# Kernel optimization log

Measured on AMD Instinct MI355X. Metric: run time of the kernel, lower is better.

Reference implementation:

```python
import jax, jax.numpy as jnp
import numpy as np

CLAMP_LO, CLAMP_HI, CLAMP_GATE_MAX = -10.0, 10.0, 10.0
E, TOPK = 8, 2
M, K, N = 2048, 2048, 1408  # tokens, hidden_dim, intermediate_dim
CAPACITY = 2 * (M * TOPK // E)


def setup_inputs() -> dict:
    key = jax.random.key(0)
    ks = jax.random.split(key, 6)
    bk = 1.0 / np.sqrt(K)  # kaiming_uniform(a=sqrt(5)) bound = 1/sqrt(fan_in)
    bn = 1.0 / np.sqrt(N)
    return {
        "flat_h": jax.random.normal(ks[0], (M, K), jnp.float32),
        "flat_idx": jax.random.randint(ks[1], (M, TOPK), 0, E),
        "flat_gate": jax.random.uniform(ks[2], (M, TOPK), jnp.float32),
        "gate_weight": jax.random.uniform(ks[3], (E, N, K), jnp.float32, -bk, bk),
        "up_weight": jax.random.uniform(ks[4], (E, N, K), jnp.float32, -bk, bk),
        "down_weight": jax.random.uniform(ks[5], (E, K, N), jnp.float32, -bn, bn),
    }


def reference(flat_h, flat_idx, flat_gate, gate_weight, up_weight, down_weight):
    m, top_k = flat_idx.shape
    k = flat_h.shape[1]
    e = gate_weight.shape[0]
    r = m * top_k

    expert_id = flat_idx.reshape(-1)                                   # (R,)
    gate = flat_gate.reshape(-1)                                       # (R,)
    token_index = jnp.repeat(jnp.arange(m, dtype=jnp.int32), top_k)    # (R,)

    # stable sort rows by expert id (mirrors torch.argsort(..., stable=True))
    sort_idx = jnp.argsort(expert_id, stable=True)
    sorted_eid = expert_id[sort_idx]
    tok_sorted = token_index[sort_idx]
    gate_sorted = gate[sort_idx]

    # position of each sorted row inside its expert group
    counts = jnp.bincount(expert_id, length=e)
    starts = jnp.concatenate([jnp.zeros(1, counts.dtype), jnp.cumsum(counts)[:-1]])
    pos = jnp.arange(r) - starts[sorted_eid]                           # (R,)

    # dispatch: scatter sorted tokens into fixed-capacity (E, C, K) buffer
    buf = jnp.zeros((e, CAPACITY, k), flat_h.dtype)
    buf = buf.at[sorted_eid, pos].set(flat_h[tok_sorted])

    # grouped GEMMs: weights stored (E, out, in) like nn.Linear
    g = jnp.einsum("eck,enk->ecn", buf, gate_weight)
    g = jnp.minimum(g, CLAMP_GATE_MAX)
    u = jnp.clip(jnp.einsum("eck,enk->ecn", buf, up_weight), CLAMP_LO, CLAMP_HI)
    h = jax.nn.silu(g) * u                                             # SwiGLU (E, C, N)
    d = jnp.einsum("ecn,ekn->eck", h, down_weight)                     # (E, C, K)

    # combine: gather each routed row back, weight by gate, sum over top_k slots
    expert_out = d[sorted_eid, pos]                                    # (R, K)
    weighted = expert_out * gate_sorted[:, None]
    out = jnp.zeros((m, k), flat_h.dtype).at[tok_sorted].add(weighted)
    return out
```

## Files before the change

### kernel.cpp

```cpp
#include <hip/hip_runtime.h>
#include <hip/hip_bf16.h>

#define M_TOK 2048
#define KDIM 2048
#define NDIM 1408
#define NEXP 8
#define RROWS (M_TOK * 2)
#define CAP 1024

typedef __attribute__((ext_vector_type(8))) short short8;
typedef __attribute__((ext_vector_type(4))) float f32x4;

__device__ __forceinline__ unsigned short bf16rn(float f) {
    unsigned int u = __builtin_bit_cast(unsigned int, f);
    u += 0x7FFFu + ((u >> 16) & 1u);
    return (unsigned short)(u >> 16);
}
__device__ __forceinline__ unsigned int pk2(float a, float b) {
    return (unsigned int)bf16rn(a) | ((unsigned int)bf16rn(b) << 16);
}
__device__ __forceinline__ unsigned int cvtpk(float a, float b) {
    __hip_bfloat162 h = __float22bfloat162_rn(make_float2(a, b));
    unsigned int u;
    __builtin_memcpy(&u, &h, 4);
    return u;
}

__device__ __forceinline__ void glds16(const void* g, void* l) {
    __builtin_amdgcn_global_load_lds(
        (const __attribute__((address_space(1))) unsigned int*)g,
        (__attribute__((address_space(3))) unsigned int*)l, 16, 0, 0);
}

__global__ void k_route(const float* __restrict__ h, const int* __restrict__ idx,
                        int* __restrict__ cnt, int* __restrict__ slot_of,
                        unsigned short* __restrict__ bufA) {
    int r = blockIdx.x;
    __shared__ int s_ep;
    if (threadIdx.x == 0) {
        int e = idx[r];
        int p = atomicAdd(&cnt[e], 1);
        int ep = e * CAP + p;
        slot_of[r] = ep;
        s_ep = ep;
    }
    __syncthreads();
    int ep = s_ep;
    const float4* src = (const float4*)(h + (size_t)(r >> 1) * KDIM) + threadIdx.x * 2;
    float4 a = src[0], b = src[1];
    uint4 o;
    o.x = pk2(a.x, a.y); o.y = pk2(a.z, a.w);
    o.z = pk2(b.x, b.y); o.w = pk2(b.z, b.w);
    *((uint4*)(bufA + (size_t)ep * KDIM) + threadIdx.x) = o;
}

__global__ __launch_bounds__(256, 2)
void k_gemm1(const unsigned short* __restrict__ bufA,
             const float* __restrict__ gw,
             const float* __restrict__ uw,
             const int* __restrict__ cnt, unsigned short* __restrict__ hbuf) {
    const int f = blockIdx.x;
    const int e = f & 7;
    const int t = f >> 3;
    const int n_blk = t % 11;
    const int m_blk = t / 11;
    const int m0 = m_blk * 128;
    if (m0 >= cnt[e]) return;
    const int n0 = n_blk * 128;

    const unsigned short* A = bufA + (size_t)e * CAP * KDIM;
    const float* G = gw + (size_t)e * NDIM * KDIM;
    const float* U = uw + (size_t)e * NDIM * KDIM;

    __shared__ unsigned short sA[128 * 64];
    __shared__ unsigned short sG[128 * 64];
    __shared__ unsigned short sU[128 * 64];

    const int tid = threadIdx.x;
    const int lane = tid & 63;
    const int wave = tid >> 6;
    const int wm = (wave >> 1) * 64, wn = (wave & 1) * 64;
    const int q = lane >> 4, l15 = lane & 15;
    const int sr = lane >> 3;
    const int scb = (lane & 7) ^ (sr & 7);
    const int xi = l15 & 7;
    const int cbl0 = (q ^ xi) * 8;
    const int cbl1 = ((4 + q) ^ xi) * 8;

    const int wrow = tid >> 1;
    const int wh = tid & 1;
    const int wx = wrow & 7;
    const float* gsrc0 = G + (size_t)(n0 + wrow) * KDIM + wh * 32;
    const float* usrc0 = U + (size_t)(n0 + wrow) * KDIM + wh * 32;
    unsigned short* wdG = &sG[wrow * 64];
    unsigned short* wdU = &sU[wrow * 64];

    f32x4 accG[4][4] = {};
    f32x4 accU[4][4] = {};

    for (int k0 = 0; k0 < KDIM; k0 += 64) {
        const float4* gs = (const float4*)(gsrc0 + k0);
        const float4* us = (const float4*)(usrc0 + k0);
        float4 gv[8], uv[8];
#pragma unroll
        for (int i = 0; i < 8; i++) gv[i] = gs[i];
#pragma unroll
        for (int i = 0; i < 8; i++) uv[i] = us[i];

        __syncthreads();
#pragma unroll
        for (int c = 0; c < 4; c++) {
            int seg = wave * 4 + c;
            int row = seg * 8 + sr;
            glds16(A + (size_t)(m0 + row) * KDIM + k0 + scb * 8, &sA[seg * 512]);
        }
#pragma unroll
        for (int g = 0; g < 4; g++) {
            uint4 o;
            o.x = cvtpk(gv[2 * g].x, gv[2 * g].y);
            o.y = cvtpk(gv[2 * g].z, gv[2 * g].w);
            o.z = cvtpk(gv[2 * g + 1].x, gv[2 * g + 1].y);
            o.w = cvtpk(gv[2 * g + 1].z, gv[2 * g + 1].w);
            *(uint4*)(wdG + (((wh * 4 + g) ^ wx) * 8)) = o;
        }
#pragma unroll
        for (int g = 0; g < 4; g++) {
            uint4 o;
            o.x = cvtpk(uv[2 * g].x, uv[2 * g].y);
            o.y = cvtpk(uv[2 * g].z, uv[2 * g].w);
            o.z = cvtpk(uv[2 * g + 1].x, uv[2 * g + 1].y);
            o.w = cvtpk(uv[2 * g + 1].z, uv[2 * g + 1].w);
            *(uint4*)(wdU + (((wh * 4 + g) ^ wx) * 8)) = o;
        }
        __syncthreads();

#pragma unroll
        for (int kh = 0; kh < 2; kh++) {
            const int co = kh ? cbl1 : cbl0;
            short8 af[4], gf[4], uf[4];
#pragma unroll
            for (int i = 0; i < 4; i++) {
                af[i] = *(const short8*)&sA[(wm + i * 16 + l15) * 64 + co];
                gf[i] = *(const short8*)&sG[(wn + i * 16 + l15) * 64 + co];
                uf[i] = *(const short8*)&sU[(wn + i * 16 + l15) * 64 + co];
            }
#pragma unroll
            for (int i = 0; i < 4; i++)
#pragma unroll
                for (int j = 0; j < 4; j++) {
                    accG[i][j] = __builtin_amdgcn_mfma_f32_16x16x32_bf16(af[i], gf[j], accG[i][j], 0, 0, 0);
                    accU[i][j] = __builtin_amdgcn_mfma_f32_16x16x32_bf16(af[i], uf[j], accU[i][j], 0, 0, 0);
                }
        }
    }

    unsigned short* H = hbuf + (size_t)e * CAP * NDIM;
#pragma unroll
    for (int i = 0; i < 4; i++)
#pragma unroll
        for (int j = 0; j < 4; j++) {
            int col = n0 + wn + j * 16 + l15;
#pragma unroll
            for (int rg = 0; rg < 4; rg++) {
                int row = m0 + wm + i * 16 + q * 4 + rg;
                float g = accG[i][j][rg];
                float u = accU[i][j][rg];
                g = fminf(g, 10.f);
                u = fminf(fmaxf(u, -10.f), 10.f);
                float hv = g / (1.f + __expf(-g)) * u;
                H[(size_t)row * NDIM + col] = bf16rn(hv);
            }
        }
}

__global__ __launch_bounds__(256, 2)
void k_gemm2(const unsigned short* __restrict__ hbuf,
             const float* __restrict__ dwn, const int* __restrict__ cnt,
             float* __restrict__ dbuf) {
    const int f = blockIdx.x;
    const int e = f & 7;
    const int t = f >> 3;
    const int n_blk = t & 15;
    const int m_blk = t >> 4;
    const int cnt_e = cnt[e];
    const int m0 = m_blk * 128;
    if (m0 >= cnt_e) return;
    const int n0 = n_blk * 128;

    const unsigned short* A = hbuf + (size_t)e * CAP * NDIM;
    const float* B = dwn + (size_t)e * KDIM * NDIM;

    __shared__ unsigned short sA[128 * 64];
    __shared__ unsigned short sB[128 * 64];

    const int tid = threadIdx.x;
    const int lane = tid & 63;
    const int wave = tid >> 6;
    const int wm = (wave >> 1) * 64, wn = (wave & 1) * 64;
    const int q = lane >> 4, l15 = lane & 15;
    const int sr = lane >> 3;
    const int scb = (lane & 7) ^ (sr & 7);
    const int xi = l15 & 7;
    const int cbl0 = (q ^ xi) * 8;
    const int cbl1 = ((4 + q) ^ xi) * 8;

    const int wrow = tid >> 1;
    const int wh = tid & 1;
    const int wx = wrow & 7;
    const float* bsrc0 = B + (size_t)(n0 + wrow) * NDIM + wh * 32;
    unsigned short* wdB = &sB[wrow * 64];

    f32x4 acc[4][4] = {};

    for (int k0 = 0; k0 < NDIM; k0 += 64) {
        const float4* bs = (const float4*)(bsrc0 + k0);
        float4 bv[8];
#pragma unroll
        for (int i = 0; i < 8; i++) bv[i] = bs[i];

        __syncthreads();
#pragma unroll
        for (int c = 0; c < 4; c++) {
            int seg = wave * 4 + c;
            int row = seg * 8 + sr;
            glds16(A + (size_t)(m0 + row) * NDIM + k0 + scb * 8, &sA[seg * 512]);
        }
#pragma unroll
        for (int g = 0; g < 4; g++) {
            uint4 o;
            o.x = cvtpk(bv[2 * g].x, bv[2 * g].y);
            o.y = cvtpk(bv[2 * g].z, bv[2 * g].w);
            o.z = cvtpk(bv[2 * g + 1].x, bv[2 * g + 1].y);
            o.w = cvtpk(bv[2 * g + 1].z, bv[2 * g + 1].w);
            *(uint4*)(wdB + (((wh * 4 + g) ^ wx) * 8)) = o;
        }
        __syncthreads();

#pragma unroll
        for (int kh = 0; kh < 2; kh++) {
            const int co = kh ? cbl1 : cbl0;
            short8 af[4], bfr[4];
#pragma unroll
            for (int i = 0; i < 4; i++) {
                af[i] = *(const short8*)&sA[(wm + i * 16 + l15) * 64 + co];
                bfr[i] = *(const short8*)&sB[(wn + i * 16 + l15) * 64 + co];
            }
#pragma unroll
            for (int i = 0; i < 4; i++)
#pragma unroll
                for (int j = 0; j < 4; j++)
                    acc[i][j] = __builtin_amdgcn_mfma_f32_16x16x32_bf16(af[i], bfr[j], acc[i][j], 0, 0, 0);
        }
    }

    float* D = dbuf + (size_t)e * CAP * KDIM;
#pragma unroll
    for (int i = 0; i < 4; i++) {
#pragma unroll
        for (int rg = 0; rg < 4; rg++) {
            int row = m0 + wm + i * 16 + q * 4 + rg;
            if (row < cnt_e) {
                float* drow = D + (size_t)row * KDIM + n0 + wn + l15;
#pragma unroll
                for (int j = 0; j < 4; j++)
                    drow[j * 16] = acc[i][j][rg];
            }
        }
    }
}

__global__ void k_combine(const float* __restrict__ dbuf, const int* __restrict__ slot_of,
                          const float* __restrict__ gate, float* __restrict__ out) {
    int tk = blockIdx.x;
    int s0 = slot_of[2 * tk], s1 = slot_of[2 * tk + 1];
    float g0 = gate[2 * tk], g1 = gate[2 * tk + 1];
    const float4* r0 = (const float4*)(dbuf + (size_t)s0 * KDIM);
    const float4* r1 = (const float4*)(dbuf + (size_t)s1 * KDIM);
    float4* o = (float4*)(out + (size_t)tk * KDIM);
    int i = threadIdx.x * 2;
#pragma unroll
    for (int c = 0; c < 2; c++) {
        float4 a = r0[i + c], b = r1[i + c];
        float4 v;
        v.x = g0 * a.x + g1 * b.x;
        v.y = g0 * a.y + g1 * b.y;
        v.z = g0 * a.z + g1 * b.z;
        v.w = g0 * a.w + g1 * b.w;
        o[i + c] = v;
    }
}

extern "C" void kernel_launch(void* const* d_in, const int* in_sizes, int n_in,
                              void* d_out, int out_size, void* d_ws, size_t ws_size,
                              hipStream_t stream) {
    const float* flat_h = (const float*)d_in[0];
    const int* flat_idx = (const int*)d_in[1];
    const float* flat_gate = (const float*)d_in[2];
    const float* gw = (const float*)d_in[3];
    const float* uw = (const float*)d_in[4];
    const float* dwn = (const float*)d_in[5];
    float* out = (float*)d_out;

    char* w = (char*)d_ws;
    int* cnt = (int*)w;
    int* slot_of = (int*)(w + 256);
    unsigned short* bufA = (unsigned short*)(w + 1048576ull);
    unsigned short* hbuf = (unsigned short*)(w + 34603008ull);
    float* dbuf = (float*)(w + 57671680ull);

    hipMemsetAsync(cnt, 0, 256, stream);

    k_route<<<RROWS, 256, 0, stream>>>(flat_h, flat_idx, cnt, slot_of, bufA);
    k_gemm1<<<8 * 11 * 8, 256, 0, stream>>>(bufA, gw, uw, cnt, hbuf);
    k_gemm2<<<8 * 16 * 8, 256, 0, stream>>>(hbuf, dwn, cnt, dbuf);
    k_combine<<<M_TOK, 256, 0, stream>>>(dbuf, slot_of, flat_gate, out);
}
```

Baseline: 531.5 us.

## Prefetch fp32 weight tiles one step ahead with coalesced row-strided loads

Both the gate/up and down GEMM kernels now load the next k-tile of fp32 weights into registers while the current tile is being consumed. The load mapping changes from two threads per row, each reading 32 contiguous floats, to 16 threads per row each reading one float4 across 8 row groups, which gives coalesced global access. Stores to shared memory become 8-byte writes into the same XOR swizzle. The aim is to hide global memory latency behind the MFMA work, at the cost of keeping register buffers live across the loop.

```diff
diff --git a/kernel.cpp b/kernel.cpp
--- a/kernel.cpp
+++ b/kernel.cpp
@@ -87,50 +87,52 @@
     const int cbl0 = (q ^ xi) * 8;
     const int cbl1 = ((4 + q) ^ xi) * 8;
 
-    const int wrow = tid >> 1;
-    const int wh = tid & 1;
-    const int wx = wrow & 7;
-    const float* gsrc0 = G + (size_t)(n0 + wrow) * KDIM + wh * 32;
-    const float* usrc0 = U + (size_t)(n0 + wrow) * KDIM + wh * 32;
-    unsigned short* wdG = &sG[wrow * 64];
-    unsigned short* wdU = &sU[wrow * 64];
+    const int row_t = tid >> 4;
+    const int c4 = tid & 15;
+    const float* Gb = G + (size_t)(n0 + row_t) * KDIM + c4 * 4;
+    const float* Ub = U + (size_t)(n0 + row_t) * KDIM + c4 * 4;
+    const int swz = (((c4 >> 1) ^ (row_t & 7)) << 3) + ((c4 & 1) << 2);
+    unsigned short* wpG = &sG[row_t * 64 + swz];
+    unsigned short* wpU = &sU[row_t * 64 + swz];
 
     f32x4 accG[4][4] = {};
     f32x4 accU[4][4] = {};
 
+    float4 gv[8], uv[8];
+#pragma unroll
+    for (int i = 0; i < 8; i++) gv[i] = *(const float4*)(Gb + (size_t)i * 16 * KDIM);
+#pragma unroll
+    for (int i = 0; i < 8; i++) uv[i] = *(const float4*)(Ub + (size_t)i * 16 * KDIM);
+
     for (int k0 = 0; k0 < KDIM; k0 += 64) {
-        const float4* gs = (const float4*)(gsrc0 + k0);
-        const float4* us = (const float4*)(usrc0 + k0);
-        float4 gv[8], uv[8];
-#pragma unroll
-        for (int i = 0; i < 8; i++) gv[i] = gs[i];
-#pragma unroll
-        for (int i = 0; i < 8; i++) uv[i] = us[i];
-
         __syncthreads();
+#pragma unroll
+        for (int i = 0; i < 8; i++) {
+            uint2 o;
+            o.x = cvtpk(gv[i].x, gv[i].y);
+            o.y = cvtpk(gv[i].z, gv[i].w);
+            *(uint2*)(wpG + i * 1024) = o;
+        }
+#pragma unroll
+        for (int i = 0; i < 8; i++) {
+            uint2 o;
+            o.x = cvtpk(uv[i].x, uv[i].y);
+            o.y = cvtpk(uv[i].z, uv[i].w);
+            *(uint2*)(wpU + i * 1024) = o;
+        }
 #pragma unroll
         for (int c = 0; c < 4; c++) {
             int seg = wave * 4 + c;
             int row = seg * 8 + sr;
             glds16(A + (size_t)(m0 + row) * KDIM + k0 + scb * 8, &sA[seg * 512]);
         }
-#pragma unroll
-        for (int g = 0; g < 4; g++) {
-            uint4 o;
-            o.x = cvtpk(gv[2 * g].x, gv[2 * g].y);
-            o.y = cvtpk(gv[2 * g].z, gv[2 * g].w);
-            o.z = cvtpk(gv[2 * g + 1].x, gv[2 * g + 1].y);
-            o.w = cvtpk(gv[2 * g + 1].z, gv[2 * g + 1].w);
-            *(uint4*)(wdG + (((wh * 4 + g) ^ wx) * 8)) = o;
-        }
-#pragma unroll
-        for (int g = 0; g < 4; g++) {
-            uint4 o;
-            o.x = cvtpk(uv[2 * g].x, uv[2 * g].y);
-            o.y = cvtpk(uv[2 * g].z, uv[2 * g].w);
-            o.z = cvtpk(uv[2 * g + 1].x, uv[2 * g + 1].y);
-            o.w = cvtpk(uv[2 * g + 1].z, uv[2 * g + 1].w);
-            *(uint4*)(wdU + (((wh * 4 + g) ^ wx) * 8)) = o;
+        if (k0 + 64 < KDIM) {
+            const float* Gn = Gb + k0 + 64;
+            const float* Un = Ub + k0 + 64;
+#pragma unroll
+            for (int i = 0; i < 8; i++) gv[i] = *(const float4*)(Gn + (size_t)i * 16 * KDIM);
+#pragma unroll
+            for (int i = 0; i < 8; i++) uv[i] = *(const float4*)(Un + (size_t)i * 16 * KDIM);
         }
         __syncthreads();
 
@@ -204,35 +206,37 @@
     const int cbl0 = (q ^ xi) * 8;
     const int cbl1 = ((4 + q) ^ xi) * 8;
 
-    const int wrow = tid >> 1;
-    const int wh = tid & 1;
-    const int wx = wrow & 7;
-    const float* bsrc0 = B + (size_t)(n0 + wrow) * NDIM + wh * 32;
-    unsigned short* wdB = &sB[wrow * 64];
+    const int row_t = tid >> 4;
+    const int c4 = tid & 15;
+    const float* Bb = B + (size_t)(n0 + row_t) * NDIM + c4 * 4;
+    const int swz = (((c4 >> 1) ^ (row_t & 7)) << 3) + ((c4 & 1) << 2);
+    unsigned short* wpB = &sB[row_t * 64 + swz];
 
     f32x4 acc[4][4] = {};
 
+    float4 bv[8];
+#pragma unroll
+    for (int i = 0; i < 8; i++) bv[i] = *(const float4*)(Bb + (size_t)i * 16 * NDIM);
+
     for (int k0 = 0; k0 < NDIM; k0 += 64) {
-        const float4* bs = (const float4*)(bsrc0 + k0);
-        float4 bv[8];
-#pragma unroll
-        for (int i = 0; i < 8; i++) bv[i] = bs[i];
-
         __syncthreads();
+#pragma unroll
+        for (int i = 0; i < 8; i++) {
+            uint2 o;
+            o.x = cvtpk(bv[i].x, bv[i].y);
+            o.y = cvtpk(bv[i].z, bv[i].w);
+            *(uint2*)(wpB + i * 1024) = o;
+        }
 #pragma unroll
         for (int c = 0; c < 4; c++) {
             int seg = wave * 4 + c;
             int row = seg * 8 + sr;
             glds16(A + (size_t)(m0 + row) * NDIM + k0 + scb * 8, &sA[seg * 512]);
         }
-#pragma unroll
-        for (int g = 0; g < 4; g++) {
-            uint4 o;
-            o.x = cvtpk(bv[2 * g].x, bv[2 * g].y);
-            o.y = cvtpk(bv[2 * g].z, bv[2 * g].w);
-            o.z = cvtpk(bv[2 * g + 1].x, bv[2 * g + 1].y);
-            o.w = cvtpk(bv[2 * g + 1].z, bv[2 * g + 1].w);
-            *(uint4*)(wdB + (((wh * 4 + g) ^ wx) * 8)) = o;
+        if (k0 + 64 < NDIM) {
+            const float* Bn = Bb + k0 + 64;
+#pragma unroll
+            for (int i = 0; i < 8; i++) bv[i] = *(const float4*)(Bn + (size_t)i * 16 * NDIM);
         }
         __syncthreads();
 
```

Result: faster. 461.4 us (-13.2%).
